# Kernel tuning notes

Measured on AMD Instinct MI355X. Metric: run time of the kernel, lower is better.

## Reference

```python
import jax, jax.numpy as jnp
import numpy as np

NEG_SLOPE = 0.2  # PyG GATConv default negative_slope
EPS = 1e-16


def gat_conv(x, src, dst, num_nodes, W, att_src, att_dst, bias, concat):
    """PyG-style GATConv (eval mode, no dropout). att_*: [H, C]."""
    H, C = att_src.shape
    h = (x @ W).reshape(num_nodes, H, C)                      # [N,H,C]
    a_s = jnp.einsum('nhc,hc->nh', h, att_src)                # [N,H]
    a_d = jnp.einsum('nhc,hc->nh', h, att_dst)                # [N,H]
    e = jax.nn.leaky_relu(a_s[src] + a_d[dst], NEG_SLOPE)     # [E,H]
    # segment softmax over edges grouped by destination node
    m = jax.lax.stop_gradient(jax.ops.segment_max(e, dst, num_segments=num_nodes))
    ex = jnp.exp(e - m[dst])
    denom = jax.ops.segment_sum(ex, dst, num_segments=num_nodes)
    alpha = ex / (denom[dst] + EPS)                           # [E,H]
    msg = h[src] * alpha[:, :, None]                          # [E,H,C]
    out = jax.ops.segment_sum(msg, dst, num_segments=num_nodes)  # [N,H,C]
    out = out.reshape(num_nodes, H * C) if concat else out.mean(axis=1)
    return out + bias


def setup_inputs() -> dict:
    key = jax.random.key(0)
    ks = jax.random.split(key, 12)
    N, E = 65536, 1310720
    IN, HID, OUT, HEADS = 768, 128, 2, 8
    C1 = HID // HEADS  # 16
    s = 0.05
    return {
        'x': jax.random.normal(ks[0], (N, IN), jnp.float32),
        'edge_index': jax.random.randint(ks[1], (2, E), 0, N, jnp.int64),
        'W1': jax.random.normal(ks[2], (IN, HEADS * C1), jnp.float32) * s,
        'att_src1': jax.random.normal(ks[3], (HEADS, C1), jnp.float32) * s,
        'att_dst1': jax.random.normal(ks[4], (HEADS, C1), jnp.float32) * s,
        'b1': jnp.zeros((HID,), jnp.float32),
        'Wp': jax.random.normal(ks[5], (IN, HID), jnp.float32) * s,
        'bp': jnp.zeros((HID,), jnp.float32),
        'W2': jax.random.normal(ks[6], (HID, OUT), jnp.float32) * s,
        'att_src2': jax.random.normal(ks[7], (1, OUT), jnp.float32) * s,
        'att_dst2': jax.random.normal(ks[8], (1, OUT), jnp.float32) * s,
        'b2': jnp.zeros((OUT,), jnp.float32),
    }


def reference(x, edge_index, W1, att_src1, att_dst1, b1, Wp, bp, W2, att_src2, att_dst2, b2):
    N = x.shape[0]
    loops = jnp.arange(N, dtype=edge_index.dtype)  # add_self_loops=True
    src = jnp.concatenate([edge_index[0], loops])
    dst = jnp.concatenate([edge_index[1], loops])
    # eval mode: dropout is identity
    h1 = gat_conv(x, src, dst, N, W1, att_src1, att_dst1, b1, concat=True)
    h = jax.nn.elu(h1 + x @ Wp + bp)  # residual projection + ELU
    return gat_conv(h, src, dst, N, W2, att_src2, att_dst2, b2, concat=False)
```

## Files before the change

### kernel.cpp

```cpp
#include <hip/hip_runtime.h>
#include <hip/hip_bf16.h>
#include <math.h>

#define NEG_SLOPE 0.2f

typedef __attribute__((ext_vector_type(8))) short short8;
typedef __attribute__((ext_vector_type(4))) float float4v;

__device__ __forceinline__ unsigned f2bf(float f) {
  unsigned u = __builtin_bit_cast(unsigned, f);
  return (u + 0x7fffu + ((u >> 16) & 1u)) >> 16;
}
__device__ __forceinline__ float bflo(unsigned u) {
  return __builtin_bit_cast(float, u << 16);
}
__device__ __forceinline__ float bfhi(unsigned u) {
  return __builtin_bit_cast(float, u & 0xffff0000u);
}

__global__ __launch_bounds__(256) void convert_w(const float* __restrict__ W1,
                                                 const float* __restrict__ Wp,
                                                 short* __restrict__ Wt) {
  int k = blockIdx.x;
  int c = threadIdx.x;
  float v = (c < 128) ? W1[k * 128 + c] : Wp[k * 128 + (c - 128)];
  Wt[(size_t)c * 768 + k] = (short)f2bf(v);
}

__global__ __launch_bounds__(256) void gemm_mfma(const float* __restrict__ x,
                                                 const short* __restrict__ Wt,
                                                 float* __restrict__ h1lin,
                                                 float* __restrict__ proj) {
  __shared__ short As[128][40];
  __shared__ short Bs[256][40];
  const int tid = threadIdx.x;
  const int wave = tid >> 6, lane = tid & 63;
  const int l15 = lane & 15, l4 = lane >> 4;
  const int row0 = blockIdx.x * 128;

  const int ar = tid >> 3;
  const int ak = (tid & 7) * 4;
  const int bc = tid >> 2;
  const int bk = (tid & 3) * 8;

  float4v acc[8][4] = {};

  for (int k0 = 0; k0 < 768; k0 += 32) {
#pragma unroll
    for (int i = 0; i < 4; i++) {
      int r = i * 32 + ar;
      float4 f = *(const float4*)&x[(size_t)(row0 + r) * 768 + k0 + ak];
      uint2 p;
      p.x = f2bf(f.x) | (f2bf(f.y) << 16);
      p.y = f2bf(f.z) | (f2bf(f.w) << 16);
      *(uint2*)&As[r][ak] = p;
    }
#pragma unroll
    for (int i = 0; i < 4; i++) {
      int c = i * 64 + bc;
      uint4 v = *(const uint4*)&Wt[(size_t)c * 768 + k0 + bk];
      *(uint4*)&Bs[c][bk] = v;
    }
    __syncthreads();

    short8 afr[8];
#pragma unroll
    for (int rt = 0; rt < 8; rt++)
      afr[rt] = *(const short8*)&As[rt * 16 + l15][l4 * 8];
#pragma unroll
    for (int ct = 0; ct < 4; ct++) {
      short8 bfr = *(const short8*)&Bs[wave * 64 + ct * 16 + l15][l4 * 8];
#pragma unroll
      for (int rt = 0; rt < 8; rt++)
        acc[rt][ct] =
            __builtin_amdgcn_mfma_f32_16x16x32_bf16(afr[rt], bfr, acc[rt][ct], 0, 0, 0);
    }
    __syncthreads();
  }

  const int colbase = wave * 64;
#pragma unroll
  for (int ct = 0; ct < 4; ct++) {
    int c = colbase + ct * 16 + l15;
    float* Cout = (c < 128) ? h1lin : proj;
    int cc = c & 127;
#pragma unroll
    for (int rt = 0; rt < 8; rt++) {
#pragma unroll
      for (int r = 0; r < 4; r++) {
        int R = row0 + rt * 16 + l4 * 4 + r;
        Cout[(size_t)R * 128 + cc] = acc[rt][ct][r];
      }
    }
  }
}

__global__ __launch_bounds__(128) void attn1(
    const float* __restrict__ h1lin, const float* __restrict__ att_src1,
    const float* __restrict__ att_dst1, float* __restrict__ a_s1,
    float* __restrict__ a_d1, unsigned* __restrict__ h1bf) {
  const int n = blockIdx.x, t = threadIdx.x;
  float v = h1lin[(size_t)n * 128 + t];
  unsigned u = f2bf(v);
  unsigned up = __shfl_xor(u, 1);
  if ((t & 1) == 0) h1bf[n * 64 + (t >> 1)] = u | (up << 16);
  float as = v * att_src1[t];
  float ad = v * att_dst1[t];
#pragma unroll
  for (int off = 8; off; off >>= 1) {
    as += __shfl_xor(as, off);
    ad += __shfl_xor(ad, off);
  }
  if ((t & 15) == 0) {
    a_s1[n * 8 + (t >> 4)] = as;
    a_d1[n * 8 + (t >> 4)] = ad;
  }
}

__global__ void init_counts(int* counts, int N) {
  int i = blockIdx.x * blockDim.x + threadIdx.x;
  if (i < N) counts[i] = 1;
}

__global__ void hist_kernel(const int* __restrict__ dst, int* counts, int E) {
  int i = blockIdx.x * blockDim.x + threadIdx.x;
  int base = i * 4;
  if (base + 3 < E) {
    int4 d = *(const int4*)&dst[base];
    atomicAdd(&counts[d.x], 1);
    atomicAdd(&counts[d.y], 1);
    atomicAdd(&counts[d.z], 1);
    atomicAdd(&counts[d.w], 1);
  } else {
    for (int j = base; j < E; j++) atomicAdd(&counts[dst[j]], 1);
  }
}

__global__ __launch_bounds__(256) void scan_a(const int* __restrict__ counts,
                                              int* offsets, int* bsum) {
  __shared__ int s[256];
  int t = threadIdx.x, idx = blockIdx.x * 256 + t;
  int v = counts[idx];
  s[t] = v;
  __syncthreads();
  for (int d = 1; d < 256; d <<= 1) {
    int x = (t >= d) ? s[t - d] : 0;
    __syncthreads();
    s[t] += x;
    __syncthreads();
  }
  offsets[idx] = s[t] - v;
  if (t == 255) bsum[blockIdx.x] = s[t];
}

__global__ __launch_bounds__(256) void scan_b(int* bsum) {
  __shared__ int s[256];
  int t = threadIdx.x;
  int v = bsum[t];
  s[t] = v;
  __syncthreads();
  for (int d = 1; d < 256; d <<= 1) {
    int x = (t >= d) ? s[t - d] : 0;
    __syncthreads();
    s[t] += x;
    __syncthreads();
  }
  bsum[t] = s[t] - v;
}

__global__ __launch_bounds__(256) void scan_c(int* offsets, const int* bsum,
                                              int* cursor, int N, int Etot) {
  int t = threadIdx.x, idx = blockIdx.x * 256 + t;
  int off = offsets[idx] + bsum[blockIdx.x];
  offsets[idx] = off;
  cursor[idx] = off;
  if (idx == 0) offsets[N] = Etot;
}

__global__ void scatter_edges(const int* __restrict__ src,
                              const int* __restrict__ dst, int* cursor,
                              int* sortedsrc, int E) {
  int i = blockIdx.x * blockDim.x + threadIdx.x;
  int base = i * 4;
  if (base + 3 < E) {
    int4 s = *(const int4*)&src[base];
    int4 d = *(const int4*)&dst[base];
    sortedsrc[atomicAdd(&cursor[d.x], 1)] = s.x;
    sortedsrc[atomicAdd(&cursor[d.y], 1)] = s.y;
    sortedsrc[atomicAdd(&cursor[d.z], 1)] = s.z;
    sortedsrc[atomicAdd(&cursor[d.w], 1)] = s.w;
  } else {
    for (int j = base; j < E; j++)
      sortedsrc[atomicAdd(&cursor[dst[j]], 1)] = src[j];
  }
}

__global__ void scatter_self(int* cursor, int* sortedsrc, int N) {
  int i = blockIdx.x * blockDim.x + threadIdx.x;
  if (i < N) {
    int pos = atomicAdd(&cursor[i], 1);
    sortedsrc[pos] = i;
  }
}

__global__ __launch_bounds__(128) void agg1_fused(
    const unsigned* __restrict__ h1bf, const float* __restrict__ proj,
    const float* __restrict__ a_s1, const float* __restrict__ a_d1,
    const int* __restrict__ offsets, const int* __restrict__ sortedsrc,
    const float* __restrict__ b1, const float* __restrict__ bp,
    const float* __restrict__ W2, const float* __restrict__ att_s2,
    const float* __restrict__ att_d2, float* __restrict__ h2,
    float* __restrict__ as2, float* __restrict__ ad2) {
  const int t = threadIdx.x;
  const int n = blockIdx.x * 4 + (t >> 5);
  const int k = t & 31;
  const int h = k >> 2;
  const float ad = a_d1[n * 8 + h];
  const int begin = offsets[n], end = offsets[n + 1];
  float acc0 = 0.f, acc1 = 0.f, acc2 = 0.f, acc3 = 0.f, aw = 0.f;
  int j = begin;
  for (; j + 2 <= end; j += 2) {
    int s0 = sortedsrc[j], s1 = sortedsrc[j + 1];
    float e0 = a_s1[s0 * 8 + h], e1 = a_s1[s1 * 8 + h];
    uint2 q0 = *(const uint2*)&h1bf[(size_t)s0 * 64 + k * 2];
    uint2 q1 = *(const uint2*)&h1bf[(size_t)s1 * 64 + k * 2];
    e0 += ad;
    e1 += ad;
    float w0 = __expf(e0 > 0.f ? e0 : NEG_SLOPE * e0);
    float w1 = __expf(e1 > 0.f ? e1 : NEG_SLOPE * e1);
    acc0 += w0 * bflo(q0.x) + w1 * bflo(q1.x);
    acc1 += w0 * bfhi(q0.x) + w1 * bfhi(q1.x);
    acc2 += w0 * bflo(q0.y) + w1 * bflo(q1.y);
    acc3 += w0 * bfhi(q0.y) + w1 * bfhi(q1.y);
    aw += w0 + w1;
  }
  if (j < end) {
    int s0 = sortedsrc[j];
    float e0 = a_s1[s0 * 8 + h] + ad;
    uint2 q0 = *(const uint2*)&h1bf[(size_t)s0 * 64 + k * 2];
    float w0 = __expf(e0 > 0.f ? e0 : NEG_SLOPE * e0);
    acc0 += w0 * bflo(q0.x);
    acc1 += w0 * bfhi(q0.x);
    acc2 += w0 * bflo(q0.y);
    acc3 += w0 * bfhi(q0.y);
    aw += w0;
  }
  const float inv = 1.f / (aw + 1e-16f);
  const float4 pj = *(const float4*)&proj[(size_t)n * 128 + k * 4];
  const float4 B1 = *(const float4*)&b1[k * 4];
  const float4 BP = *(const float4*)&bp[k * 4];
  float v0 = acc0 * inv + pj.x + B1.x + BP.x;
  float v1 = acc1 * inv + pj.y + B1.y + BP.y;
  float v2 = acc2 * inv + pj.z + B1.z + BP.z;
  float v3 = acc3 * inv + pj.w + B1.w + BP.w;
  v0 = v0 > 0.f ? v0 : (__expf(v0) - 1.f);
  v1 = v1 > 0.f ? v1 : (__expf(v1) - 1.f);
  v2 = v2 > 0.f ? v2 : (__expf(v2) - 1.f);
  v3 = v3 > 0.f ? v3 : (__expf(v3) - 1.f);
  float2 w20 = *(const float2*)&W2[(k * 4 + 0) * 2];
  float2 w21 = *(const float2*)&W2[(k * 4 + 1) * 2];
  float2 w22 = *(const float2*)&W2[(k * 4 + 2) * 2];
  float2 w23 = *(const float2*)&W2[(k * 4 + 3) * 2];
  float p0 = v0 * w20.x + v1 * w21.x + v2 * w22.x + v3 * w23.x;
  float p1 = v0 * w20.y + v1 * w21.y + v2 * w22.y + v3 * w23.y;
#pragma unroll
  for (int off = 16; off; off >>= 1) {
    p0 += __shfl_xor(p0, off);
    p1 += __shfl_xor(p1, off);
  }
  if (k == 0) {
    h2[2 * n] = p0;
    h2[2 * n + 1] = p1;
    as2[n] = p0 * att_s2[0] + p1 * att_s2[1];
    ad2[n] = p0 * att_d2[0] + p1 * att_d2[1];
  }
}

__global__ __launch_bounds__(256) void agg2(
    const float* __restrict__ h2, const float* __restrict__ as2,
    const float* __restrict__ ad2, const int* __restrict__ offsets,
    const int* __restrict__ sortedsrc, const float* __restrict__ b2,
    float* __restrict__ out, int N) {
  const int node = blockIdx.x * 16 + (threadIdx.x >> 4);
  const int lane = threadIdx.x & 15;
  const int begin = offsets[node], end = offsets[node + 1];
  const float ad = ad2[node];
  float acc0 = 0.f, acc1 = 0.f, aw = 0.f;
  for (int j = begin + lane; j < end; j += 16) {
    int s = sortedsrc[j];
    float e = as2[s] + ad;
    float w = __expf(e > 0.f ? e : NEG_SLOPE * e);
    float2 hh = *(const float2*)&h2[2 * s];
    acc0 += w * hh.x;
    acc1 += w * hh.y;
    aw += w;
  }
#pragma unroll
  for (int off = 8; off; off >>= 1) {
    acc0 += __shfl_xor(acc0, off);
    acc1 += __shfl_xor(acc1, off);
    aw += __shfl_xor(aw, off);
  }
  if (lane == 0) {
    float inv = 1.f / (aw + 1e-16f);
    out[2 * node] = acc0 * inv + b2[0];
    out[2 * node + 1] = acc1 * inv + b2[1];
  }
}

extern "C" void kernel_launch(void* const* d_in, const int* in_sizes, int n_in,
                              void* d_out, int out_size, void* d_ws,
                              size_t ws_size, hipStream_t stream) {
  const float* x = (const float*)d_in[0];
  const int* edge_index = (const int*)d_in[1];
  const float* W1 = (const float*)d_in[2];
  const float* att_src1 = (const float*)d_in[3];
  const float* att_dst1 = (const float*)d_in[4];
  const float* b1 = (const float*)d_in[5];
  const float* Wp = (const float*)d_in[6];
  const float* bp = (const float*)d_in[7];
  const float* W2 = (const float*)d_in[8];
  const float* att_src2 = (const float*)d_in[9];
  const float* att_dst2 = (const float*)d_in[10];
  const float* b2 = (const float*)d_in[11];
  float* out = (float*)d_out;

  const int N = in_sizes[0] / 768;
  const int E = in_sizes[1] / 2;
  const int Etot = E + N;
  const int* src = edge_index;
  const int* dst = edge_index + E;

  char* ws = (char*)d_ws;
  size_t off = 0;
  auto alloc = [&](size_t bytes) {
    size_t cur = off;
    off += (bytes + 255) & ~(size_t)255;
    return (void*)(ws + cur);
  };
  float* h1lin = (float*)alloc((size_t)N * 128 * 4);
  float* proj = (float*)alloc((size_t)N * 128 * 4);
  unsigned* h1bf = (unsigned*)alloc((size_t)N * 64 * 4);
  float* a_s1 = (float*)alloc((size_t)N * 8 * 4);
  float* a_d1 = (float*)alloc((size_t)N * 8 * 4);
  float* h2 = (float*)alloc((size_t)N * 2 * 4);
  float* as2 = (float*)alloc((size_t)N * 4);
  float* ad2 = (float*)alloc((size_t)N * 4);
  int* counts = (int*)alloc((size_t)N * 4);
  int* offsets = (int*)alloc(((size_t)N + 1) * 4);
  int* cursor = (int*)alloc((size_t)N * 4);
  int* bsum = (int*)alloc(256 * 4);
  int* sortedsrc = (int*)alloc((size_t)Etot * 4);
  short* Wt = (short*)alloc((size_t)256 * 768 * 2);

  convert_w<<<768, 256, 0, stream>>>(W1, Wp, Wt);
  gemm_mfma<<<N / 128, 256, 0, stream>>>(x, Wt, h1lin, proj);
  attn1<<<N, 128, 0, stream>>>(h1lin, att_src1, att_dst1, a_s1, a_d1, h1bf);
  init_counts<<<(N + 255) / 256, 256, 0, stream>>>(counts, N);
  hist_kernel<<<(E / 4 + 255) / 256, 256, 0, stream>>>(dst, counts, E);
  scan_a<<<N / 256, 256, 0, stream>>>(counts, offsets, bsum);
  scan_b<<<1, 256, 0, stream>>>(bsum);
  scan_c<<<N / 256, 256, 0, stream>>>(offsets, bsum, cursor, N, Etot);
  scatter_edges<<<(E / 4 + 255) / 256, 256, 0, stream>>>(src, dst, cursor,
                                                         sortedsrc, E);
  scatter_self<<<(N + 255) / 256, 256, 0, stream>>>(cursor, sortedsrc, N);
  agg1_fused<<<N / 4, 128, 0, stream>>>(h1bf, proj, a_s1, a_d1, offsets,
                                        sortedsrc, b1, bp, W2, att_src2,
                                        att_dst2, h2, as2, ad2);
  agg2<<<N / 16, 256, 0, stream>>>(h2, as2, ad2, offsets, sortedsrc, b2, out,
                                   N);
}
```

Measured before the change: 584.8 us.

## Fuse attention-score epilogue into GEMM, fold self-loops into scan, widen aggregation

The GEMM epilogue now writes bf16 h1 and computes the per-head source and destination attention scores directly. This removes the fp32 h1lin buffer and the separate attn1 kernel. Self-loop edges are placed in the scan_c kernel instead of a separate atomic scatter kernel. The first-layer aggregation now uses 16 lanes per node with 16-byte bf16 gathers and a 4-edge unroll, which raises memory-level parallelism but adds register pressure and more shuffles in the GEMM epilogue.

```diff
diff --git a/kernel.cpp b/kernel.cpp
--- a/kernel.cpp
+++ b/kernel.cpp
@@ -27,10 +27,11 @@
   Wt[(size_t)c * 768 + k] = (short)f2bf(v);
 }
 
-__global__ __launch_bounds__(256) void gemm_mfma(const float* __restrict__ x,
-                                                 const short* __restrict__ Wt,
-                                                 float* __restrict__ h1lin,
-                                                 float* __restrict__ proj) {
+__global__ __launch_bounds__(256) void gemm_mfma(
+    const float* __restrict__ x, const short* __restrict__ Wt,
+    const float* __restrict__ att_src1, const float* __restrict__ att_dst1,
+    float* __restrict__ proj, unsigned* __restrict__ h1bf,
+    float* __restrict__ a_s1, float* __restrict__ a_d1) {
   __shared__ short As[128][40];
   __shared__ short Bs[256][40];
   const int tid = threadIdx.x;
@@ -79,41 +80,48 @@
   }
 
   const int colbase = wave * 64;
-#pragma unroll
-  for (int ct = 0; ct < 4; ct++) {
-    int c = colbase + ct * 16 + l15;
-    float* Cout = (c < 128) ? h1lin : proj;
-    int cc = c & 127;
-#pragma unroll
-    for (int rt = 0; rt < 8; rt++) {
-#pragma unroll
-      for (int r = 0; r < 4; r++) {
-        int R = row0 + rt * 16 + l4 * 4 + r;
-        Cout[(size_t)R * 128 + cc] = acc[rt][ct][r];
+  if (wave < 2) {
+#pragma unroll
+    for (int ct = 0; ct < 4; ct++) {
+      const int c = colbase + ct * 16 + l15;
+      const int head = wave * 4 + ct;
+      const float asw = att_src1[c];
+      const float adw = att_dst1[c];
+#pragma unroll
+      for (int rt = 0; rt < 8; rt++) {
+#pragma unroll
+        for (int r = 0; r < 4; r++) {
+          const int R = row0 + rt * 16 + l4 * 4 + r;
+          const float v = acc[rt][ct][r];
+          unsigned u = f2bf(v);
+          unsigned up = __shfl_xor(u, 1);
+          if ((l15 & 1) == 0) h1bf[(size_t)R * 64 + (c >> 1)] = u | (up << 16);
+          float as = v * asw, ad = v * adw;
+#pragma unroll
+          for (int off = 8; off; off >>= 1) {
+            as += __shfl_xor(as, off);
+            ad += __shfl_xor(ad, off);
+          }
+          if (l15 == 0) {
+            a_s1[R * 8 + head] = as;
+            a_d1[R * 8 + head] = ad;
+          }
+        }
       }
     }
-  }
-}
-
-__global__ __launch_bounds__(128) void attn1(
-    const float* __restrict__ h1lin, const float* __restrict__ att_src1,
-    const float* __restrict__ att_dst1, float* __restrict__ a_s1,
-    float* __restrict__ a_d1, unsigned* __restrict__ h1bf) {
-  const int n = blockIdx.x, t = threadIdx.x;
-  float v = h1lin[(size_t)n * 128 + t];
-  unsigned u = f2bf(v);
-  unsigned up = __shfl_xor(u, 1);
-  if ((t & 1) == 0) h1bf[n * 64 + (t >> 1)] = u | (up << 16);
-  float as = v * att_src1[t];
-  float ad = v * att_dst1[t];
-#pragma unroll
-  for (int off = 8; off; off >>= 1) {
-    as += __shfl_xor(as, off);
-    ad += __shfl_xor(ad, off);
-  }
-  if ((t & 15) == 0) {
-    a_s1[n * 8 + (t >> 4)] = as;
-    a_d1[n * 8 + (t >> 4)] = ad;
+  } else {
+#pragma unroll
+    for (int ct = 0; ct < 4; ct++) {
+      const int c = colbase - 128 + ct * 16 + l15;
+#pragma unroll
+      for (int rt = 0; rt < 8; rt++) {
+#pragma unroll
+        for (int r = 0; r < 4; r++) {
+          const int R = row0 + rt * 16 + l4 * 4 + r;
+          proj[(size_t)R * 128 + c] = acc[rt][ct][r];
+        }
+      }
+    }
   }
 }
 
@@ -169,11 +177,13 @@
 }
 
 __global__ __launch_bounds__(256) void scan_c(int* offsets, const int* bsum,
-                                              int* cursor, int N, int Etot) {
+                                              int* cursor, int* sortedsrc,
+                                              int N, int Etot) {
   int t = threadIdx.x, idx = blockIdx.x * 256 + t;
   int off = offsets[idx] + bsum[blockIdx.x];
   offsets[idx] = off;
-  cursor[idx] = off;
+  sortedsrc[off] = idx;
+  cursor[idx] = off + 1;
   if (idx == 0) offsets[N] = Etot;
 }
 
@@ -195,16 +205,8 @@
   }
 }
 
-__global__ void scatter_self(int* cursor, int* sortedsrc, int N) {
-  int i = blockIdx.x * blockDim.x + threadIdx.x;
-  if (i < N) {
-    int pos = atomicAdd(&cursor[i], 1);
-    sortedsrc[pos] = i;
-  }
-}
-
-__global__ __launch_bounds__(128) void agg1_fused(
-    const unsigned* __restrict__ h1bf, const float* __restrict__ proj,
+__global__ __launch_bounds__(256) void agg1_fused(
+    const uint4* __restrict__ h1bf4, const float* __restrict__ proj,
     const float* __restrict__ a_s1, const float* __restrict__ a_d1,
     const int* __restrict__ offsets, const int* __restrict__ sortedsrc,
     const float* __restrict__ b1, const float* __restrict__ bp,
@@ -212,59 +214,79 @@
     const float* __restrict__ att_d2, float* __restrict__ h2,
     float* __restrict__ as2, float* __restrict__ ad2) {
   const int t = threadIdx.x;
-  const int n = blockIdx.x * 4 + (t >> 5);
-  const int k = t & 31;
-  const int h = k >> 2;
-  const float ad = a_d1[n * 8 + h];
+  const int n = blockIdx.x * 16 + (t >> 4);
+  const int k = t & 15;
+  const int hd = k >> 1;
+  const float ad = a_d1[n * 8 + hd];
   const int begin = offsets[n], end = offsets[n + 1];
-  float acc0 = 0.f, acc1 = 0.f, acc2 = 0.f, acc3 = 0.f, aw = 0.f;
+  float acc[8] = {};
+  float aw = 0.f;
   int j = begin;
-  for (; j + 2 <= end; j += 2) {
+  for (; j + 4 <= end; j += 4) {
     int s0 = sortedsrc[j], s1 = sortedsrc[j + 1];
-    float e0 = a_s1[s0 * 8 + h], e1 = a_s1[s1 * 8 + h];
-    uint2 q0 = *(const uint2*)&h1bf[(size_t)s0 * 64 + k * 2];
-    uint2 q1 = *(const uint2*)&h1bf[(size_t)s1 * 64 + k * 2];
-    e0 += ad;
-    e1 += ad;
+    int s2 = sortedsrc[j + 2], s3 = sortedsrc[j + 3];
+    float e0 = a_s1[s0 * 8 + hd], e1 = a_s1[s1 * 8 + hd];
+    float e2 = a_s1[s2 * 8 + hd], e3 = a_s1[s3 * 8 + hd];
+    uint4 q0 = h1bf4[(size_t)s0 * 16 + k];
+    uint4 q1 = h1bf4[(size_t)s1 * 16 + k];
+    uint4 q2 = h1bf4[(size_t)s2 * 16 + k];
+    uint4 q3 = h1bf4[(size_t)s3 * 16 + k];
+    e0 += ad; e1 += ad; e2 += ad; e3 += ad;
     float w0 = __expf(e0 > 0.f ? e0 : NEG_SLOPE * e0);
     float w1 = __expf(e1 > 0.f ? e1 : NEG_SLOPE * e1);
-    acc0 += w0 * bflo(q0.x) + w1 * bflo(q1.x);
-    acc1 += w0 * bfhi(q0.x) + w1 * bfhi(q1.x);
-    acc2 += w0 * bflo(q0.y) + w1 * bflo(q1.y);
-    acc3 += w0 * bfhi(q0.y) + w1 * bfhi(q1.y);
-    aw += w0 + w1;
-  }
-  if (j < end) {
+    float w2 = __expf(e2 > 0.f ? e2 : NEG_SLOPE * e2);
+    float w3 = __expf(e3 > 0.f ? e3 : NEG_SLOPE * e3);
+    acc[0] += w0 * bflo(q0.x) + w1 * bflo(q1.x) + w2 * bflo(q2.x) + w3 * bflo(q3.x);
+    acc[1] += w0 * bfhi(q0.x) + w1 * bfhi(q1.x) + w2 * bfhi(q2.x) + w3 * bfhi(q3.x);
+    acc[2] += w0 * bflo(q0.y) + w1 * bflo(q1.y) + w2 * bflo(q2.y) + w3 * bflo(q3.y);
+    acc[3] += w0 * bfhi(q0.y) + w1 * bfhi(q1.y) + w2 * bfhi(q2.y) + w3 * bfhi(q3.y);
+    acc[4] += w0 * bflo(q0.z) + w1 * bflo(q1.z) + w2 * bflo(q2.z) + w3 * bflo(q3.z);
+    acc[5] += w0 * bfhi(q0.z) + w1 * bfhi(q1.z) + w2 * bfhi(q2.z) + w3 * bfhi(q3.z);
+    acc[6] += w0 * bflo(q0.w) + w1 * bflo(q1.w) + w2 * bflo(q2.w) + w3 * bflo(q3.w);
+    acc[7] += w0 * bfhi(q0.w) + w1 * bfhi(q1.w) + w2 * bfhi(q2.w) + w3 * bfhi(q3.w);
+    aw += (w0 + w1) + (w2 + w3);
+  }
+  for (; j < end; j++) {
     int s0 = sortedsrc[j];
-    float e0 = a_s1[s0 * 8 + h] + ad;
-    uint2 q0 = *(const uint2*)&h1bf[(size_t)s0 * 64 + k * 2];
+    float e0 = a_s1[s0 * 8 + hd] + ad;
+    uint4 q0 = h1bf4[(size_t)s0 * 16 + k];
     float w0 = __expf(e0 > 0.f ? e0 : NEG_SLOPE * e0);
-    acc0 += w0 * bflo(q0.x);
-    acc1 += w0 * bfhi(q0.x);
-    acc2 += w0 * bflo(q0.y);
-    acc3 += w0 * bfhi(q0.y);
+    acc[0] += w0 * bflo(q0.x);
+    acc[1] += w0 * bfhi(q0.x);
+    acc[2] += w0 * bflo(q0.y);
+    acc[3] += w0 * bfhi(q0.y);
+    acc[4] += w0 * bflo(q0.z);
+    acc[5] += w0 * bfhi(q0.z);
+    acc[6] += w0 * bflo(q0.w);
+    acc[7] += w0 * bfhi(q0.w);
     aw += w0;
   }
   const float inv = 1.f / (aw + 1e-16f);
-  const float4 pj = *(const float4*)&proj[(size_t)n * 128 + k * 4];
-  const float4 B1 = *(const float4*)&b1[k * 4];
-  const float4 BP = *(const float4*)&bp[k * 4];
-  float v0 = acc0 * inv + pj.x + B1.x + BP.x;
-  float v1 = acc1 * inv + pj.y + B1.y + BP.y;
-  float v2 = acc2 * inv + pj.z + B1.z + BP.z;
-  float v3 = acc3 * inv + pj.w + B1.w + BP.w;
-  v0 = v0 > 0.f ? v0 : (__expf(v0) - 1.f);
-  v1 = v1 > 0.f ? v1 : (__expf(v1) - 1.f);
-  v2 = v2 > 0.f ? v2 : (__expf(v2) - 1.f);
-  v3 = v3 > 0.f ? v3 : (__expf(v3) - 1.f);
-  float2 w20 = *(const float2*)&W2[(k * 4 + 0) * 2];
-  float2 w21 = *(const float2*)&W2[(k * 4 + 1) * 2];
-  float2 w22 = *(const float2*)&W2[(k * 4 + 2) * 2];
-  float2 w23 = *(const float2*)&W2[(k * 4 + 3) * 2];
-  float p0 = v0 * w20.x + v1 * w21.x + v2 * w22.x + v3 * w23.x;
-  float p1 = v0 * w20.y + v1 * w21.y + v2 * w22.y + v3 * w23.y;
-#pragma unroll
-  for (int off = 16; off; off >>= 1) {
+  const float4 pj0 = *(const float4*)&proj[(size_t)n * 128 + k * 8];
+  const float4 pj1 = *(const float4*)&proj[(size_t)n * 128 + k * 8 + 4];
+  const float4 b1a = *(const float4*)&b1[k * 8];
+  const float4 b1b = *(const float4*)&b1[k * 8 + 4];
+  const float4 bpa = *(const float4*)&bp[k * 8];
+  const float4 bpb = *(const float4*)&bp[k * 8 + 4];
+  float v[8];
+  v[0] = acc[0] * inv + pj0.x + b1a.x + bpa.x;
+  v[1] = acc[1] * inv + pj0.y + b1a.y + bpa.y;
+  v[2] = acc[2] * inv + pj0.z + b1a.z + bpa.z;
+  v[3] = acc[3] * inv + pj0.w + b1a.w + bpa.w;
+  v[4] = acc[4] * inv + pj1.x + b1b.x + bpb.x;
+  v[5] = acc[5] * inv + pj1.y + b1b.y + bpb.y;
+  v[6] = acc[6] * inv + pj1.z + b1b.z + bpb.z;
+  v[7] = acc[7] * inv + pj1.w + b1b.w + bpb.w;
+  float p0 = 0.f, p1 = 0.f;
+#pragma unroll
+  for (int i = 0; i < 8; i++) {
+    float vi = v[i] > 0.f ? v[i] : (__expf(v[i]) - 1.f);
+    float2 w2 = *(const float2*)&W2[(k * 8 + i) * 2];
+    p0 += vi * w2.x;
+    p1 += vi * w2.y;
+  }
+#pragma unroll
+  for (int off = 8; off; off >>= 1) {
     p0 += __shfl_xor(p0, off);
     p1 += __shfl_xor(p1, off);
   }
@@ -338,7 +360,6 @@
     off += (bytes + 255) & ~(size_t)255;
     return (void*)(ws + cur);
   };
-  float* h1lin = (float*)alloc((size_t)N * 128 * 4);
   float* proj = (float*)alloc((size_t)N * 128 * 4);
   unsigned* h1bf = (unsigned*)alloc((size_t)N * 64 * 4);
   float* a_s1 = (float*)alloc((size_t)N * 8 * 4);
@@ -354,19 +375,19 @@
   short* Wt = (short*)alloc((size_t)256 * 768 * 2);
 
   convert_w<<<768, 256, 0, stream>>>(W1, Wp, Wt);
-  gemm_mfma<<<N / 128, 256, 0, stream>>>(x, Wt, h1lin, proj);
-  attn1<<<N, 128, 0, stream>>>(h1lin, att_src1, att_dst1, a_s1, a_d1, h1bf);
+  gemm_mfma<<<N / 128, 256, 0, stream>>>(x, Wt, att_src1, att_dst1, proj, h1bf,
+                                         a_s1, a_d1);
   init_counts<<<(N + 255) / 256, 256, 0, stream>>>(counts, N);
   hist_kernel<<<(E / 4 + 255) / 256, 256, 0, stream>>>(dst, counts, E);
   scan_a<<<N / 256, 256, 0, stream>>>(counts, offsets, bsum);
   scan_b<<<1, 256, 0, stream>>>(bsum);
-  scan_c<<<N / 256, 256, 0, stream>>>(offsets, bsum, cursor, N, Etot);
+  scan_c<<<N / 256, 256, 0, stream>>>(offsets, bsum, cursor, sortedsrc, N,
+                                      Etot);
   scatter_edges<<<(E / 4 + 255) / 256, 256, 0, stream>>>(src, dst, cursor,
                                                          sortedsrc, E);
-  scatter_self<<<(N + 255) / 256, 256, 0, stream>>>(cursor, sortedsrc, N);
-  agg1_fused<<<N / 4, 128, 0, stream>>>(h1bf, proj, a_s1, a_d1, offsets,
-                                        sortedsrc, b1, bp, W2, att_src2,
-                                        att_dst2, h2, as2, ad2);
+  agg1_fused<<<N / 16, 256, 0, stream>>>((const uint4*)h1bf, proj, a_s1, a_d1,
+                                         offsets, sortedsrc, b1, bp, W2,
+                                         att_src2, att_dst2, h2, as2, ad2);
   agg2<<<N / 16, 256, 0, stream>>>(h2, as2, ad2, offsets, sortedsrc, b2, out,
                                    N);
 }
```

Measured after the change: 612.6 us. +4.8%, slower.
